# Optimization experiments

Hardware: AMD Instinct MI355X
Metric: run time of the kernel (lower is better)

The kernel has to match this reference:

```python
import jax, jax.numpy as jnp
import numpy as np

N, D, E, K, CAP = 16384, 1024, 64, 2, 640

def setup_inputs() -> dict:
    key = jax.random.key(0)
    k1, k2, k3 = jax.random.split(key, 3)
    x = jax.random.normal(k1, (N, D), dtype=jnp.float32)
    Wr = jax.random.normal(k2, (D, E), dtype=jnp.float32) / np.sqrt(D)
    br = jnp.zeros((E,), dtype=jnp.float32)
    We = jax.random.normal(k3, (E, D, D), dtype=jnp.float32) / np.sqrt(D)
    return {"x": x, "Wr": Wr, "br": br, "We": We, "k": K, "capacity": CAP}

def _route(x, Wr, br, k, num_experts):
    logits = x @ Wr + br                                  # [N, E]
    top_k_vals, top_k_idxs = jax.lax.top_k(logits, k)     # [N, k]
    gates = jax.nn.softmax(top_k_vals, axis=-1)           # [N, k]
    # flatten k-major like the original: transpose((1,0)).flatten()
    flat = top_k_idxs.T.reshape(-1)                       # [k*N]
    expert_mask = (flat[:, None] == jnp.arange(num_experts)).astype(jnp.int32)
    buffer_idxs = jnp.cumsum(expert_mask, axis=0) * expert_mask - 1  # [k*N, E]
    buffer_idxs = buffer_idxs.reshape(k, -1, num_experts)            # [k, N, E]
    dispatch_idxs = buffer_idxs.transpose(2, 0, 1).max(axis=1)       # [E, N]
    combine_idxs = buffer_idxs.max(axis=-1).T                        # [N, k]
    return gates, top_k_idxs, dispatch_idxs, combine_idxs

def reference(x, Wr, br, We, k, capacity):
    num_experts = Wr.shape[1]
    gates, top_k_idxs, dispatch_idxs, combine_idxs = _route(x, Wr, br, k, num_experts)
    # dispatch: scatter tokens into per-expert capacity buffers; unassigned (-1)
    # and overflow (>= capacity) tokens land in the dropped slot `capacity`.
    d_idx = jnp.where((dispatch_idxs < 0) | (dispatch_idxs > capacity), capacity, dispatch_idxs)
    def scatter_one(idx):
        return jnp.zeros((capacity + 1, x.shape[-1]), x.dtype).at[idx].set(x)[:-1]
    dispatched = jax.vmap(scatter_one)(d_idx)             # [E, C, D]
    # per-expert linear (the wrap()/vmap-ed expert), grouped GEMM
    expert_out = jax.nn.relu(jnp.einsum('ecd,edh->ech', dispatched, We))
    # combine: gather back, pad row `capacity` yields zeros for dropped tokens
    padded = jnp.pad(expert_out, ((0, 0), (0, 1), (0, 0)))
    c_idx = jnp.where((combine_idxs < 0) | (combine_idxs > capacity), capacity, combine_idxs)
    combined = padded[top_k_idxs, c_idx]                  # [N, k, D]
    return jnp.einsum('nk,nkd->nd', gates, combined)      # [N, D]
```

## Files before the change

kernel.cpp:

```cpp
#include <hip/hip_runtime.h>
#include <hip/hip_bf16.h>
#include <cstdint>
#include <cstddef>

#define N_TOK 16384
#define DIM   1024
#define NEXP  64
#define CAPACITY 640

typedef __bf16 bf16x8 __attribute__((ext_vector_type(8)));
typedef float  f32x4  __attribute__((ext_vector_type(4)));

__device__ __forceinline__ unsigned short f2bf(float f) {
    union { float f; unsigned int u; } a; a.f = f;
    unsigned int r = a.u + 0x7FFFu + ((a.u >> 16) & 1u);
    return (unsigned short)(r >> 16);
}

__global__ __launch_bounds__(256) void router_convert(
    const float* __restrict__ x, const float* __restrict__ Wr,
    const float* __restrict__ br, const float* __restrict__ We,
    unsigned short* __restrict__ xb, unsigned short* __restrict__ WeB,
    int* __restrict__ top2i, float* __restrict__ gates2,
    int* __restrict__ hist, float* __restrict__ out)
{
    __shared__ __align__(16) float smem[2][64][68];
    const int tid = threadIdx.x;

    if (blockIdx.x >= 8448) {
        const int z = blockIdx.x - 8448;
        float4* o = (float4*)(out + (size_t)z * 32768);
        const float4 zero = make_float4(0.f, 0.f, 0.f, 0.f);
#pragma unroll
        for (int l = 0; l < 32; l++) o[l * 256 + tid] = zero;
        return;
    }

    if (blockIdx.x >= 256) {
        const int b   = blockIdx.x - 256;
        const int e   = b >> 7;
        const int nt  = (b >> 4) & 7;
        const int ksi = b & 15;
        unsigned short (*T)[132] = (unsigned short (*)[132])smem;
        const int tc  = (tid & 31) * 4;
        const int tr  = tid >> 5;
        const float* src = We + ((size_t)e << 20) + (size_t)(ksi * 64) * DIM + nt * 128;
#pragma unroll
        for (int l = 0; l < 8; l++) {
            int dr = l * 8 + tr;
            float4 v = *(const float4*)(src + (size_t)dr * DIM + tc);
            ushort4 u = make_ushort4(f2bf(v.x), f2bf(v.y), f2bf(v.z), f2bf(v.w));
            *(ushort4*)&T[dr][tc] = u;
        }
        __syncthreads();
        unsigned short* dst = WeB + ((size_t)b << 13);
#pragma unroll
        for (int i = 0; i < 4; i++) {
            int p = i * 256 + tid;
            int kq = p >> 7, col = p & 127;
            unsigned int w0 = (unsigned int)T[kq * 8 + 0][col] | ((unsigned int)T[kq * 8 + 1][col] << 16);
            unsigned int w1 = (unsigned int)T[kq * 8 + 2][col] | ((unsigned int)T[kq * 8 + 3][col] << 16);
            unsigned int w2 = (unsigned int)T[kq * 8 + 4][col] | ((unsigned int)T[kq * 8 + 5][col] << 16);
            unsigned int w3 = (unsigned int)T[kq * 8 + 6][col] | ((unsigned int)T[kq * 8 + 7][col] << 16);
            *(uint4*)(dst + (size_t)p * 8) = make_uint4(w0, w1, w2, w3);
        }
        return;
    }

    float (*xs)[68] = smem[0];
    float (*wT)[68] = smem[1];
    const int t0  = blockIdx.x * 64;
    const int tm  = tid >> 4;
    const int te  = tid & 15;

    float acc[4][4];
#pragma unroll
    for (int i = 0; i < 4; i++)
#pragma unroll
        for (int j = 0; j < 4; j++) acc[i][j] = 0.f;

    for (int ks = 0; ks < DIM; ks += 64) {
        __syncthreads();
#pragma unroll
        for (int l = 0; l < 4; l++) {
            int row = l * 16 + tm;
            int col = te * 4;
            float4 v = *(const float4*)(x + (size_t)(t0 + row) * DIM + ks + col);
            *(float4*)&xs[row][col] = v;
            ushort4 b = make_ushort4(f2bf(v.x), f2bf(v.y), f2bf(v.z), f2bf(v.w));
            *(ushort4*)(xb + (size_t)(t0 + row) * DIM + ks + col) = b;
        }
#pragma unroll
        for (int l = 0; l < 4; l++) {
            int kr = l * 16 + tm;
            int ec = te * 4;
            float4 v = *(const float4*)(Wr + (size_t)(ks + kr) * NEXP + ec);
            wT[ec + 0][kr] = v.x; wT[ec + 1][kr] = v.y;
            wT[ec + 2][kr] = v.z; wT[ec + 3][kr] = v.w;
        }
        __syncthreads();
#pragma unroll 4
        for (int kk = 0; kk < 64; kk += 4) {
            float4 xv[4], wv[4];
#pragma unroll
            for (int i = 0; i < 4; i++) xv[i] = *(float4*)&xs[tm + i * 16][kk];
#pragma unroll
            for (int j = 0; j < 4; j++) wv[j] = *(float4*)&wT[te + j * 16][kk];
#pragma unroll
            for (int i = 0; i < 4; i++)
#pragma unroll
                for (int j = 0; j < 4; j++)
                    acc[i][j] += xv[i].x * wv[j].x + xv[i].y * wv[j].y +
                                 xv[i].z * wv[j].z + xv[i].w * wv[j].w;
        }
    }
    __syncthreads();
#pragma unroll
    for (int i = 0; i < 4; i++)
#pragma unroll
        for (int j = 0; j < 4; j++)
            xs[tm + i * 16][te + j * 16] = acc[i][j] + br[te + j * 16];
    __syncthreads();
    if (tid < 64) {
        int n = t0 + tid;
        float v1 = -1e30f, v2 = -1e30f; int i1 = 0, i2 = 0;
        for (int e = 0; e < 64; e++) {
            float v = xs[tid][e];
            if (v > v1)      { v2 = v1; i2 = i1; v1 = v; i1 = e; }
            else if (v > v2) { v2 = v;  i2 = e; }
        }
        float g0 = 1.f / (1.f + expf(v2 - v1));
        top2i[n * 2 + 0] = i1; top2i[n * 2 + 1] = i2;
        gates2[n * 2 + 0] = g0; gates2[n * 2 + 1] = 1.f - g0;
        atomicAdd(&hist[(n >> 8) * NEXP + i1], 1);
        atomicAdd(&hist[(64 + (n >> 8)) * NEXP + i2], 1);
    }
}

__global__ __launch_bounds__(64) void rank_kernel(
    const int* __restrict__ top2i, const float* __restrict__ gates2,
    const int* __restrict__ hist, int* __restrict__ list_tok,
    float* __restrict__ list_gate, int* __restrict__ cntc,
    int* __restrict__ slot_of)
{
    int lane = threadIdx.x;
    int c = blockIdx.x;
    int cnt_reg = 0;
#pragma unroll 4
    for (int cc = 0; cc < c; cc++) cnt_reg += hist[cc * NEXP + lane];
    unsigned long long below = (1ull << lane) - 1ull;
    for (int r = 0; r < 4; r++) {
        int p = c * 256 + r * 64 + lane;
        int k = p >> 14, n = p & 16383;
        int e = top2i[n * 2 + k];
        int slot = 0;
#pragma unroll 1
        for (int q = 0; q < NEXP; q++) {
            unsigned long long mask = __ballot(e == q);
            int base = __shfl(cnt_reg, q);
            if (e == q) slot = base + __popcll(mask & below);
            if (lane == q) cnt_reg += (int)__popcll(mask);
        }
        slot_of[p] = slot;
        if (slot < CAPACITY) {
            list_tok[e * CAPACITY + slot]  = n | (k << 16);
            list_gate[e * CAPACITY + slot] = gates2[n * 2 + k];
        }
    }
    if (c == 127) cntc[lane] = cnt_reg < CAPACITY ? cnt_reg : CAPACITY;
}

template <int MODE>
__global__ __launch_bounds__(256) void moe_gemm3t(
    const unsigned short* __restrict__ xb, const unsigned short* __restrict__ WeB,
    const int* __restrict__ list_tok, const float* __restrict__ list_gate,
    const int* __restrict__ cntc, float* __restrict__ outc)
{
    const int bid = blockIdx.x;
    const int e   = bid / 40;
    const int rem = bid % 40;
    const int mt  = rem >> 3;
    const int nt  = rem & 7;
    const int cnt = cntc[e];
    if (mt * 128 >= cnt) return;
    int valid = cnt - mt * 128; if (valid > 128) valid = 128;

    __shared__ __align__(16) unsigned short As[2][8192];
    __shared__ __align__(16) unsigned short Bs[2][8192];
    __shared__ int   tok_s[128];
    __shared__ int   crow_s[128];
    __shared__ float gate_s[128];

    const int tid = threadIdx.x;
    if (tid < 128) {
        int slot = mt * 128 + tid;
        bool v = tid < valid;
        int raw = v ? list_tok[e * CAPACITY + slot] : list_tok[e * CAPACITY];
        int n   = raw & 0x3FFF;
        tok_s[tid]  = n;
        crow_s[tid] = ((raw >> 16) << 14) | n;
        gate_s[tid] = v ? list_gate[e * CAPACITY + slot] : 0.f;
    }
    __syncthreads();

    const int arow  = tid & 127;
    const int ahalf = tid >> 7;
    const unsigned short* aG = xb + (size_t)tok_s[arow] * DIM + ahalf * 8;
    const unsigned short* bG = WeB + ((size_t)(e * 8 + nt) * 16) * 8192 + (size_t)tid * 8;

    const int wv   = tid >> 6;
    const int lane = tid & 63;
    const int wm = wv >> 1, wn = wv & 1;
    const int fm = lane & 15, kq = lane >> 4;

    f32x4 acc[4][4];
#pragma unroll
    for (int i = 0; i < 4; i++)
#pragma unroll
        for (int j = 0; j < 4; j++) acc[i][j] = (f32x4){0.f, 0.f, 0.f, 0.f};

    auto stage = [&](int buf, int ksi) {
#pragma unroll
        for (int i = 0; i < 4; i++) {
            const int ldsOff = (i * 256 + wv * 64) * 8;
            __builtin_amdgcn_global_load_lds(
                (const __attribute__((address_space(1))) unsigned int*)(aG + ksi * 64 + i * 16),
                (__attribute__((address_space(3))) unsigned int*)(&As[buf][ldsOff]), 16, 0, 0);
            __builtin_amdgcn_global_load_lds(
                (const __attribute__((address_space(1))) unsigned int*)(bG + (size_t)ksi * 8192 + i * 2048),
                (__attribute__((address_space(3))) unsigned int*)(&Bs[buf][ldsOff]), 16, 0, 0);
        }
    };
    auto compute = [&](int buf) {
#pragma unroll
        for (int kk = 0; kk < 2; kk++) {
            union { uint4 u; bf16x8 v; } fa[4], fb[4];
#pragma unroll
            for (int i = 0; i < 4; i++)
                fa[i].u = *(const uint4*)(&As[buf][((kk * 4 + kq) * 128 + wm * 64 + i * 16 + fm) * 8]);
#pragma unroll
            for (int j = 0; j < 4; j++)
                fb[j].u = *(const uint4*)(&Bs[buf][((kk * 4 + kq) * 128 + wn * 64 + j * 16 + fm) * 8]);
#pragma unroll
            for (int i = 0; i < 4; i++)
#pragma unroll
                for (int j = 0; j < 4; j++)
                    acc[i][j] = __builtin_amdgcn_mfma_f32_16x16x32_bf16(
                        fa[i].v, fb[j].v, acc[i][j], 0, 0, 0);
        }
    };

    stage(0, 0);
    __syncthreads();
    int cur = 0;
#pragma unroll 1
    for (int ksi = 1; ksi < 16; ksi++) {
        stage(cur ^ 1, ksi);
        compute(cur);
        __syncthreads();
        cur ^= 1;
    }
    compute(cur);

    const int col0 = nt * 128 + wn * 64 + fm;
#pragma unroll
    for (int i = 0; i < 4; i++) {
        int rbase = wm * 64 + i * 16 + kq * 4;
#pragma unroll
        for (int j = 0; j < 4; j++) {
            int col = col0 + j * 16;
#pragma unroll
            for (int r = 0; r < 4; r++) {
                int row = rbase + r;
                if (row < valid) {
                    float v = acc[i][j][r];
                    v = fmaxf(v, 0.f) * gate_s[row];
                    if (MODE == 0)
                        atomicAdd(outc + (size_t)tok_s[row] * DIM + col, v);
                    else
                        outc[(size_t)crow_s[row] * DIM + col] = v;
                }
            }
        }
    }
}

__global__ __launch_bounds__(256) void combine_kernel(
    const float* __restrict__ comb, const int* __restrict__ slot_of,
    float* __restrict__ out)
{
    const int n = blockIdx.x;
    const int d = threadIdx.x;
    const int s0 = slot_of[n];
    const int s1 = slot_of[N_TOK + n];
    float4 r = make_float4(0.f, 0.f, 0.f, 0.f);
    if (s0 < CAPACITY) {
        float4 v = ((const float4*)(comb + (size_t)n * DIM))[d];
        r.x = v.x; r.y = v.y; r.z = v.z; r.w = v.w;
    }
    if (s1 < CAPACITY) {
        float4 v = ((const float4*)(comb + ((size_t)N_TOK + n) * DIM))[d];
        r.x += v.x; r.y += v.y; r.z += v.z; r.w += v.w;
    }
    ((float4*)(out + (size_t)n * DIM))[d] = r;
}

#define MT 128
#define NT 128
#define BK 32
#define LDA 36

__global__ __launch_bounds__(256) void moe_gemm(
    const unsigned short* __restrict__ xb, const float* __restrict__ We,
    const int* __restrict__ list_tok, const float* __restrict__ list_gate,
    const int* __restrict__ cntc, float* __restrict__ out)
{
    const int bid = blockIdx.x;
    const int e   = bid / 40;
    const int rem = bid % 40;
    const int mt  = rem >> 3;
    const int nt  = rem & 7;
    const int cnt = cntc[e];
    if (mt * MT >= cnt) return;
    int valid = cnt - mt * MT; if (valid > MT) valid = MT;

    __shared__ unsigned short As[MT * LDA];
    __shared__ unsigned short Bs[NT * LDA];
    __shared__ int   tok_s[MT];
    __shared__ float gate_s[MT];

    const int tid = threadIdx.x;
    if (tid < MT) {
        int slot = mt * MT + tid;
        bool v = tid < valid;
        int raw = v ? list_tok[e * CAPACITY + slot] : list_tok[e * CAPACITY];
        tok_s[tid]  = raw & 0x3FFF;
        gate_s[tid] = v ? list_gate[e * CAPACITY + slot] : 0.f;
    }
    __syncthreads();

    const int arow = tid >> 1, ah = tid & 1;
    const unsigned short* aptr = xb + (size_t)tok_s[arow] * DIM + ah * 16;
    const int bn0 = (tid & 31) * 4;
    const int bkr = (tid >> 5) * 4;
    const float* bptr = We + (size_t)e * DIM * DIM + (size_t)bkr * DIM + nt * NT + bn0;

    f32x4 acc[4][4];
#pragma unroll
    for (int i = 0; i < 4; i++)
#pragma unroll
        for (int j = 0; j < 4; j++) acc[i][j] = (f32x4){0.f, 0.f, 0.f, 0.f};

    const int lane = tid & 63, wave = tid >> 6;
    const int wm = wave >> 1, wn = wave & 1;
    const int fm = lane & 15, kq = lane >> 4;

    for (int ks = 0; ks < DIM; ks += BK) {
        __syncthreads();
        uint4 a0 = *(const uint4*)(aptr + ks);
        uint4 a1 = *(const uint4*)(aptr + ks + 8);
        {
            unsigned short* d = &As[arow * LDA + ah * 16];
            *(uint2*)(d + 0)  = make_uint2(a0.x, a0.y);
            *(uint2*)(d + 4)  = make_uint2(a0.z, a0.w);
            *(uint2*)(d + 8)  = make_uint2(a1.x, a1.y);
            *(uint2*)(d + 12) = make_uint2(a1.z, a1.w);
        }
        {
            float4 b[4];
#pragma unroll
            for (int j = 0; j < 4; j++)
                b[j] = *(const float4*)(bptr + (size_t)(ks + j) * DIM);
            union { float4 v; float f[4]; } u0, u1, u2, u3;
            u0.v = b[0]; u1.v = b[1]; u2.v = b[2]; u3.v = b[3];
#pragma unroll
            for (int cc = 0; cc < 4; cc++) {
                unsigned int lo = (unsigned int)f2bf(u0.f[cc]) | ((unsigned int)f2bf(u1.f[cc]) << 16);
                unsigned int hi = (unsigned int)f2bf(u2.f[cc]) | ((unsigned int)f2bf(u3.f[cc]) << 16);
                *(uint2*)&Bs[(bn0 + cc) * LDA + bkr] = make_uint2(lo, hi);
            }
        }
        __syncthreads();
        union { uint2 u[2]; bf16x8 v; } fa[4], fb[4];
#pragma unroll
        for (int i = 0; i < 4; i++) {
            const unsigned short* s = &As[(wm * 64 + i * 16 + fm) * LDA + kq * 8];
            fa[i].u[0] = *(const uint2*)(s);
            fa[i].u[1] = *(const uint2*)(s + 4);
        }
#pragma unroll
        for (int j = 0; j < 4; j++) {
            const unsigned short* s = &Bs[(wn * 64 + j * 16 + fm) * LDA + kq * 8];
            fb[j].u[0] = *(const uint2*)(s);
            fb[j].u[1] = *(const uint2*)(s + 4);
        }
#pragma unroll
        for (int i = 0; i < 4; i++)
#pragma unroll
            for (int j = 0; j < 4; j++)
                acc[i][j] = __builtin_amdgcn_mfma_f32_16x16x32_bf16(
                    fa[i].v, fb[j].v, acc[i][j], 0, 0, 0);
    }

    const int col0 = nt * NT + wn * 64 + fm;
#pragma unroll
    for (int i = 0; i < 4; i++) {
        int rbase = wm * 64 + i * 16 + kq * 4;
#pragma unroll
        for (int j = 0; j < 4; j++) {
            int col = col0 + j * 16;
#pragma unroll
            for (int r = 0; r < 4; r++) {
                int row = rbase + r;
                if (row < valid) {
                    float v = acc[i][j][r];
                    v = fmaxf(v, 0.f) * gate_s[row];
                    atomicAdd(out + (size_t)tok_s[row] * DIM + col, v);
                }
            }
        }
    }
}

extern "C" void kernel_launch(void* const* d_in, const int* in_sizes, int n_in,
                              void* d_out, int out_size, void* d_ws, size_t ws_size,
                              hipStream_t stream)
{
    const float* x  = (const float*)d_in[0];
    const float* Wr = (const float*)d_in[1];
    const float* br = (const float*)d_in[2];
    const float* We = (const float*)d_in[3];
    float* out = (float*)d_out;

    char* ws = (char*)d_ws;
    size_t off = 0;
    unsigned short* xb = (unsigned short*)(ws + off); off += (size_t)N_TOK * DIM * 2;
    int*   top2i     = (int*)(ws + off);   off += (size_t)N_TOK * 2 * 4;
    float* gates2    = (float*)(ws + off); off += (size_t)N_TOK * 2 * 4;
    int*   hist      = (int*)(ws + off);   off += 128 * NEXP * 4;
    int*   cntc      = (int*)(ws + off);   off += NEXP * 4;
    int*   list_tok  = (int*)(ws + off);   off += NEXP * CAPACITY * 4;
    float* list_gate = (float*)(ws + off); off += NEXP * CAPACITY * 4;
    int*   slot_of   = (int*)(ws + off);   off += (size_t)N_TOK * 2 * 4;
    off = (off + 255) & ~(size_t)255;
    unsigned short* WeB = (unsigned short*)(ws + off);
    size_t need = off + (size_t)NEXP * DIM * DIM * 2;
    size_t off2 = (need + 255) & ~(size_t)255;
    float* comb = (float*)(ws + off2);
    size_t need2 = off2 + (size_t)N_TOK * 2 * DIM * 4;

    const bool fast2 = ws_size >= need2;
    const bool fast  = ws_size >= need;

    hipMemsetAsync(hist, 0, 128 * NEXP * 4, stream);
    if (fast2) {
        router_convert<<<8448, 256, 0, stream>>>(x, Wr, br, We, xb, WeB,
                                                 top2i, gates2, hist, out);
        rank_kernel<<<128, 64, 0, stream>>>(top2i, gates2, hist,
                                            list_tok, list_gate, cntc, slot_of);
        moe_gemm3t<1><<<NEXP * 40, 256, 0, stream>>>(xb, WeB, list_tok,
                                                     list_gate, cntc, comb);
        combine_kernel<<<N_TOK, 256, 0, stream>>>(comb, slot_of, out);
    } else if (fast) {
        router_convert<<<8960, 256, 0, stream>>>(x, Wr, br, We, xb, WeB,
                                                 top2i, gates2, hist, out);
        rank_kernel<<<128, 64, 0, stream>>>(top2i, gates2, hist,
                                            list_tok, list_gate, cntc, slot_of);
        moe_gemm3t<0><<<NEXP * 40, 256, 0, stream>>>(xb, WeB, list_tok,
                                                     list_gate, cntc, out);
    } else {
        hipMemsetAsync(out, 0, (size_t)N_TOK * DIM * 4, stream);
        router_convert<<<256, 256, 0, stream>>>(x, Wr, br, We, xb, xb,
                                                top2i, gates2, hist, out);
        rank_kernel<<<128, 64, 0, stream>>>(top2i, gates2, hist,
                                            list_tok, list_gate, cntc, slot_of);
        moe_gemm<<<NEXP * 40, 256, 0, stream>>>(xb, We, list_tok, list_gate,
                                                cntc, out);
    }
}
```

Baseline: 678.1 us.

## Replace histogram ranking with per-expert scan; deepen GEMM prefetch pipeline and remap blocks

Removes the router's atomic histogram and the hist memset, and replaces the serial 128-block ballot ranking with one block per expert. Each block counts matches, prefix-scans them in shared memory and assigns slots in token order. The grouped GEMM now keeps two K-stages in flight, using explicit vmcnt waits and raw barriers instead of a stage-then-sync loop, and its block index is remapped so consecutive blocks spread across experts. The new ranking reads all of top2i once per expert, 64 times in total, which could cost more than the old scheme. The hand-placed waitcnt values also depend on how many loads each stage issues.

```diff
diff --git a/kernel.cpp b/kernel.cpp
--- a/kernel.cpp
+++ b/kernel.cpp
@@ -22,7 +22,7 @@
     const float* __restrict__ br, const float* __restrict__ We,
     unsigned short* __restrict__ xb, unsigned short* __restrict__ WeB,
     int* __restrict__ top2i, float* __restrict__ gates2,
-    int* __restrict__ hist, float* __restrict__ out)
+    float* __restrict__ out)
 {
     __shared__ __align__(16) float smem[2][64][68];
     const int tid = threadIdx.x;
@@ -132,51 +132,61 @@
         float g0 = 1.f / (1.f + expf(v2 - v1));
         top2i[n * 2 + 0] = i1; top2i[n * 2 + 1] = i2;
         gates2[n * 2 + 0] = g0; gates2[n * 2 + 1] = 1.f - g0;
-        atomicAdd(&hist[(n >> 8) * NEXP + i1], 1);
-        atomicAdd(&hist[(64 + (n >> 8)) * NEXP + i2], 1);
-    }
-}
-
-__global__ __launch_bounds__(64) void rank_kernel(
+    }
+}
+
+__global__ __launch_bounds__(256) void rank2(
     const int* __restrict__ top2i, const float* __restrict__ gates2,
-    const int* __restrict__ hist, int* __restrict__ list_tok,
-    float* __restrict__ list_gate, int* __restrict__ cntc,
-    int* __restrict__ slot_of)
-{
-    int lane = threadIdx.x;
-    int c = blockIdx.x;
-    int cnt_reg = 0;
+    int* __restrict__ list_tok, float* __restrict__ list_gate,
+    int* __restrict__ cntc, int* __restrict__ slot_of)
+{
+    const int e   = blockIdx.x;
+    const int tid = threadIdx.x;
+    __shared__ int scan_s[256];
+
+    const int p0 = tid * 128;
+    const int k  = p0 >> 14;
+    const int n0 = p0 & 16383;
+
+    int cnt = 0;
 #pragma unroll 4
-    for (int cc = 0; cc < c; cc++) cnt_reg += hist[cc * NEXP + lane];
-    unsigned long long below = (1ull << lane) - 1ull;
-    for (int r = 0; r < 4; r++) {
-        int p = c * 256 + r * 64 + lane;
-        int k = p >> 14, n = p & 16383;
-        int e = top2i[n * 2 + k];
-        int slot = 0;
+    for (int q = 0; q < 128; q++)
+        cnt += (top2i[(n0 + q) * 2 + k] == e);
+
+    scan_s[tid] = cnt;
+    __syncthreads();
+    for (int d = 1; d < 256; d <<= 1) {
+        int add = (tid >= d) ? scan_s[tid - d] : 0;
+        __syncthreads();
+        scan_s[tid] += add;
+        __syncthreads();
+    }
+    int base  = scan_s[tid] - cnt;
+    int total = scan_s[255];
+
 #pragma unroll 1
-        for (int q = 0; q < NEXP; q++) {
-            unsigned long long mask = __ballot(e == q);
-            int base = __shfl(cnt_reg, q);
-            if (e == q) slot = base + __popcll(mask & below);
-            if (lane == q) cnt_reg += (int)__popcll(mask);
-        }
-        slot_of[p] = slot;
-        if (slot < CAPACITY) {
-            list_tok[e * CAPACITY + slot]  = n | (k << 16);
-            list_gate[e * CAPACITY + slot] = gates2[n * 2 + k];
-        }
-    }
-    if (c == 127) cntc[lane] = cnt_reg < CAPACITY ? cnt_reg : CAPACITY;
+    for (int q = 0; q < 128; q++) {
+        int p = p0 + q;
+        int n = n0 + q;
+        if (top2i[n * 2 + k] == e) {
+            int slot = base++;
+            slot_of[p] = slot;
+            if (slot < CAPACITY) {
+                list_tok[e * CAPACITY + slot]  = n | (k << 16);
+                list_gate[e * CAPACITY + slot] = gates2[n * 2 + k];
+            }
+        }
+    }
+    if (tid == 0) cntc[e] = total < CAPACITY ? total : CAPACITY;
 }
 
 template <int MODE>
-__global__ __launch_bounds__(256) void moe_gemm3t(
+__global__ __launch_bounds__(256) void moe_gemm4(
     const unsigned short* __restrict__ xb, const unsigned short* __restrict__ WeB,
     const int* __restrict__ list_tok, const float* __restrict__ list_gate,
     const int* __restrict__ cntc, float* __restrict__ outc)
 {
-    const int bid = blockIdx.x;
+    const int bid = (blockIdx.x & 7) * 320 + (blockIdx.x >> 3);
     const int e   = bid / 40;
     const int rem = bid % 40;
     const int mt  = rem >> 3;
@@ -251,16 +261,26 @@
     };
 
     stage(0, 0);
-    __syncthreads();
-    int cur = 0;
+    stage(1, 1);
 #pragma unroll 1
-    for (int ksi = 1; ksi < 16; ksi++) {
-        stage(cur ^ 1, ksi);
-        compute(cur);
-        __syncthreads();
-        cur ^= 1;
-    }
-    compute(cur);
+    for (int t = 0; t < 14; t++) {
+        asm volatile("s_waitcnt vmcnt(8)" ::: "memory");
+        __builtin_amdgcn_s_barrier();
+        __builtin_amdgcn_sched_barrier(0);
+        compute(t & 1);
+        __builtin_amdgcn_s_barrier();
+        __builtin_amdgcn_sched_barrier(0);
+        stage(t & 1, t + 2);
+    }
+    asm volatile("s_waitcnt vmcnt(8)" ::: "memory");
+    __builtin_amdgcn_s_barrier();
+    __builtin_amdgcn_sched_barrier(0);
+    compute(0);
+    __builtin_amdgcn_s_barrier();
+    asm volatile("s_waitcnt vmcnt(0)" ::: "memory");
+    __builtin_amdgcn_s_barrier();
+    __builtin_amdgcn_sched_barrier(0);
+    compute(1);
 
     const int col0 = nt * 128 + wn * 64 + fm;
 #pragma unroll
@@ -437,7 +457,6 @@
     unsigned short* xb = (unsigned short*)(ws + off); off += (size_t)N_TOK * DIM * 2;
     int*   top2i     = (int*)(ws + off);   off += (size_t)N_TOK * 2 * 4;
     float* gates2    = (float*)(ws + off); off += (size_t)N_TOK * 2 * 4;
-    int*   hist      = (int*)(ws + off);   off += 128 * NEXP * 4;
     int*   cntc      = (int*)(ws + off);   off += NEXP * 4;
     int*   list_tok  = (int*)(ws + off);   off += NEXP * CAPACITY * 4;
     float* list_gate = (float*)(ws + off); off += NEXP * CAPACITY * 4;
@@ -452,28 +471,27 @@
     const bool fast2 = ws_size >= need2;
     const bool fast  = ws_size >= need;
 
-    hipMemsetAsync(hist, 0, 128 * NEXP * 4, stream);
     if (fast2) {
         router_convert<<<8448, 256, 0, stream>>>(x, Wr, br, We, xb, WeB,
-                                                 top2i, gates2, hist, out);
-        rank_kernel<<<128, 64, 0, stream>>>(top2i, gates2, hist,
-                                            list_tok, list_gate, cntc, slot_of);
-        moe_gemm3t<1><<<NEXP * 40, 256, 0, stream>>>(xb, WeB, list_tok,
-                                                     list_gate, cntc, comb);
+                                                 top2i, gates2, out);
+        rank2<<<NEXP, 256, 0, stream>>>(top2i, gates2,
+                                        list_tok, list_gate, cntc, slot_of);
+        moe_gemm4<1><<<NEXP * 40, 256, 0, stream>>>(xb, WeB, list_tok,
+                                                    list_gate, cntc, comb);
         combine_kernel<<<N_TOK, 256, 0, stream>>>(comb, slot_of, out);
     } else if (fast) {
         router_convert<<<8960, 256, 0, stream>>>(x, Wr, br, We, xb, WeB,
-                                                 top2i, gates2, hist, out);
-        rank_kernel<<<128, 64, 0, stream>>>(top2i, gates2, hist,
-                                            list_tok, list_gate, cntc, slot_of);
-        moe_gemm3t<0><<<NEXP * 40, 256, 0, stream>>>(xb, WeB, list_tok,
-                                                     list_gate, cntc, out);
+                                                 top2i, gates2, out);
+        rank2<<<NEXP, 256, 0, stream>>>(top2i, gates2,
+                                        list_tok, list_gate, cntc, slot_of);
+        moe_gemm4<0><<<NEXP * 40, 256, 0, stream>>>(xb, WeB, list_tok,
+                                                    list_gate, cntc, out);
     } else {
         hipMemsetAsync(out, 0, (size_t)N_TOK * DIM * 4, stream);
         router_convert<<<256, 256, 0, stream>>>(x, Wr, br, We, xb, xb,
-                                                top2i, gates2, hist, out);
-        rank_kernel<<<128, 64, 0, stream>>>(top2i, gates2, hist,
-                                            list_tok, list_gate, cntc, slot_of);
+                                                top2i, gates2, out);
+        rank2<<<NEXP, 256, 0, stream>>>(top2i, gates2,
+                                        list_tok, list_gate, cntc, slot_of);
         moe_gemm<<<NEXP * 40, 256, 0, stream>>>(xb, We, list_tok, list_gate,
                                                 cntc, out);
     }
```

After: 710.0 us. 1.05x slower.
